# Kernel optimization log

Measured on AMD Instinct MI355X. Metric: run time of the kernel, lower is better.

The kernel has to match this reference:

```python
import jax, jax.numpy as jnp
import numpy as np

L = 512          # angles_max_length
R_CA = 3.8       # C-alpha - C-alpha virtual bond length (AB model)


def _B_mat(a, b):
    # Rigid transform of the AB C-alpha model: rot(alpha) about z, rot(beta), translate R along x.
    ca, sa = jnp.cos(a), jnp.sin(a)
    cb, sb = jnp.cos(b), jnp.sin(b)
    z = jnp.zeros_like(a)
    o = jnp.ones_like(a)
    rows = [
        [ca, -sa * cb,  sa * sb, R_CA * ca],
        [sa,  ca * cb, -ca * sb, R_CA * sa],
        [z,   sb,       cb,      z],
        [z,   z,        z,       o],
    ]
    return jnp.stack([jnp.stack(r, -1) for r in rows], -2)  # (..., 4, 4)


def _dB_da(a, b):
    ca, sa = jnp.cos(a), jnp.sin(a)
    cb, sb = jnp.cos(b), jnp.sin(b)
    z = jnp.zeros_like(a)
    rows = [
        [-sa, -ca * cb,  ca * sb, -R_CA * sa],
        [ ca, -sa * cb,  sa * sb,  R_CA * ca],
        [z, z, z, z],
        [z, z, z, z],
    ]
    return jnp.stack([jnp.stack(r, -1) for r in rows], -2)


def _dB_db(a, b):
    ca, sa = jnp.cos(a), jnp.sin(a)
    cb, sb = jnp.cos(b), jnp.sin(b)
    z = jnp.zeros_like(a)
    rows = [
        [z,  sa * sb,  sa * cb, z],
        [z, -ca * sb, -ca * cb, z],
        [z,  cb,      -sb,      z],
        [z, z, z, z],
    ]
    return jnp.stack([jnp.stack(r, -1) for r in rows], -2)


def setup_inputs() -> dict:
    key = jax.random.key(0)
    k1, k2, k3 = jax.random.split(key, 3)
    input_angles = jax.random.normal(k1, (32, 2, L), dtype=jnp.float32)
    input_coords = jax.random.normal(k2, (32, 3 * (L + 1)), dtype=jnp.float32)
    angles_length = jax.random.randint(k3, (32,), 0, L, dtype=jnp.int32)
    return {"input_angles": input_angles, "input_coords": input_coords,
            "angles_length": angles_length}


def reference(input_angles, input_coords, angles_length):
    Bsz = input_angles.shape[0]
    alpha = input_angles[:, 0, :]  # (B, L)
    beta = input_angles[:, 1, :]

    Bm = _B_mat(alpha, beta)  # (B, L, 4, 4)
    # Prefix products M_i = B_0 @ ... @ B_i (order-preserving associative scan).
    M = jax.lax.associative_scan(lambda x, y: x @ y, Bm, axis=1)
    eye = jnp.broadcast_to(jnp.eye(4, dtype=Bm.dtype), (Bsz, 1, 4, 4))
    M_prev = jnp.concatenate([eye, M[:, :-1]], axis=1)  # M_{i-1}

    # Rigid-transform inverse of M_i: [R^T, -R^T t; 0 1]
    Rm = M[..., :3, :3]
    t = M[..., :3, 3:]
    Rt = jnp.swapaxes(Rm, -1, -2)
    bottom = jnp.broadcast_to(jnp.array([0., 0., 0., 1.], Bm.dtype), (Bsz, L, 1, 4))
    Minv = jnp.concatenate(
        [jnp.concatenate([Rt, -(Rt @ t)], axis=-1), bottom], axis=-2)

    # F_i^q = M_{i-1} dB_i/dq M_i^{-1};  dr_j/dq_i = F_i^q r_j^h  (for j > i)
    Fa = M_prev @ _dB_da(alpha, beta) @ Minv  # (B, L, 4, 4)
    Fb = M_prev @ _dB_db(alpha, beta) @ Minv

    coords = input_coords.reshape(Bsz, L + 1, 3)
    rh = jnp.concatenate([coords, jnp.ones((Bsz, L + 1, 1), coords.dtype)], -1)

    ga = jnp.einsum('blij,bmj->blmi', Fa, rh)[..., :3]  # (B, L, L+1, 3)
    gb = jnp.einsum('blij,bmj->blmi', Fb, rh)[..., :3]

    i = jnp.arange(L)[:, None]
    j = jnp.arange(L + 1)[None, :]
    lens = angles_length[:, None, None]
    mask = ((j > i) & (i < lens) & (j <= lens))[..., None]
    ga = jnp.where(mask, ga, 0.0)
    gb = jnp.where(mask, gb, 0.0)

    out = jnp.stack([ga, gb], axis=1)  # (B, 2, L, L+1, 3)
    return out.reshape(Bsz, 2, 3 * L * (L + 1))
```

## Files before the change

kernel.cpp:

```cpp
#include <hip/hip_runtime.h>

#define LSEQ 512
#define RCA 3.8f

typedef float f32x4 __attribute__((ext_vector_type(4)));

struct Aff { float m[3][4]; };

__device__ __forceinline__ Aff compose(const Aff& A, const Aff& B) {
    Aff C;
#pragma unroll
    for (int i = 0; i < 3; ++i) {
#pragma unroll
        for (int j = 0; j < 4; ++j) {
            float v = A.m[i][0] * B.m[0][j] + A.m[i][1] * B.m[1][j] + A.m[i][2] * B.m[2][j];
            if (j == 3) v += A.m[i][3];
            C.m[i][j] = v;
        }
    }
    return C;
}

__device__ __forceinline__ Aff shflUp(const Aff& a, int d) {
    Aff r;
#pragma unroll
    for (int i = 0; i < 3; ++i)
#pragma unroll
        for (int j = 0; j < 4; ++j)
            r.m[i][j] = __shfl_up(a.m[i][j], d, 64);
    return r;
}

__device__ __forceinline__ Aff makeB(float ca, float sa, float cb, float sb) {
    Aff B;
    B.m[0][0] = ca;  B.m[0][1] = -sa * cb; B.m[0][2] =  sa * sb; B.m[0][3] = RCA * ca;
    B.m[1][0] = sa;  B.m[1][1] =  ca * cb; B.m[1][2] = -ca * sb; B.m[1][3] = RCA * sa;
    B.m[2][0] = 0.f; B.m[2][1] =  sb;      B.m[2][2] =  cb;      B.m[2][3] = 0.f;
    return B;
}

__global__ __launch_bounds__(512) void scan_kernel(const float* __restrict__ angles,
                                                   float* __restrict__ F) {
    const int b = blockIdx.x;
    const int tid = threadIdx.x;
    const int lane = tid & 63;
    const int w = tid >> 6;

    __shared__ float sT[8][12];

    const float a  = angles[(size_t)b * 1024 + tid];
    const float be = angles[(size_t)b * 1024 + 512 + tid];
    float sa, ca, sb, cb;
    sincosf(a, &sa, &ca);
    sincosf(be, &sb, &cb);

    Aff S = makeB(ca, sa, cb, sb);
#pragma unroll
    for (int d = 1; d < 64; d <<= 1) {
        Aff o = shflUp(S, d);
        if (lane >= d) S = compose(o, S);
    }

    if (lane == 63) {
#pragma unroll
        for (int k = 0; k < 12; ++k) sT[w][k] = S.m[k / 4][k % 4];
    }
    __syncthreads();

    Aff E;
#pragma unroll
    for (int i = 0; i < 3; ++i)
#pragma unroll
        for (int j = 0; j < 4; ++j) E.m[i][j] = (i == j) ? 1.f : 0.f;
    for (int k = 0; k < w; ++k) {
        Aff T;
#pragma unroll
        for (int q = 0; q < 12; ++q) T.m[q / 4][q % 4] = sT[k][q];
        E = compose(E, T);
    }

    const Aff Sp = shflUp(S, 1);
    const Aff M = compose(E, S);
    Aff Mprev;
    if (lane == 0) Mprev = E;
    else           Mprev = compose(E, Sp);

    float Rt[3][3], ti[3];
#pragma unroll
    for (int i = 0; i < 3; ++i)
#pragma unroll
        for (int j = 0; j < 3; ++j) Rt[i][j] = M.m[j][i];
#pragma unroll
    for (int i = 0; i < 3; ++i)
        ti[i] = -(M.m[0][i] * M.m[0][3] + M.m[1][i] * M.m[1][3] + M.m[2][i] * M.m[2][3]);

    float d0[4] = {-sa, -ca * cb,  ca * sb, -RCA * sa};
    float d1[4] = { ca, -sa * cb,  sa * sb,  RCA * ca};
    float e01 =  sa * sb, e02 =  sa * cb;
    float e11 = -ca * sb, e12 = -ca * cb;
    float e21 =  cb,      e22 = -sb;

    float Ga[3][4], Gb[3][4];
#pragma unroll
    for (int i = 0; i < 3; ++i) {
        float p0 = Mprev.m[i][0], p1 = Mprev.m[i][1], p2 = Mprev.m[i][2];
#pragma unroll
        for (int j = 0; j < 4; ++j) Ga[i][j] = p0 * d0[j] + p1 * d1[j];
        Gb[i][0] = 0.f;
        Gb[i][1] = p0 * e01 + p1 * e11 + p2 * e21;
        Gb[i][2] = p0 * e02 + p1 * e12 + p2 * e22;
        Gb[i][3] = 0.f;
    }

    float W[24];
#pragma unroll
    for (int i = 0; i < 3; ++i) {
#pragma unroll
        for (int j = 0; j < 3; ++j) {
            W[i * 4 + j]      = Ga[i][0] * Rt[0][j] + Ga[i][1] * Rt[1][j] + Ga[i][2] * Rt[2][j];
            W[12 + i * 4 + j] = Gb[i][0] * Rt[0][j] + Gb[i][1] * Rt[1][j] + Gb[i][2] * Rt[2][j];
        }
        W[i * 4 + 3]      = Ga[i][0] * ti[0] + Ga[i][1] * ti[1] + Ga[i][2] * ti[2] + Ga[i][3];
        W[12 + i * 4 + 3] = Gb[i][0] * ti[0] + Gb[i][1] * ti[1] + Gb[i][2] * ti[2] + Gb[i][3];
    }

    f32x4* w4 = reinterpret_cast<f32x4*>(F + ((size_t)b * LSEQ + tid) * 24);
    const f32x4* s4 = reinterpret_cast<const f32x4*>(W);
#pragma unroll
    for (int q = 0; q < 6; ++q) w4[q] = s4[q];
}

__global__ __launch_bounds__(256) void emit_kernel(const float* __restrict__ F,
                                                   const float* __restrict__ coords,
                                                   const int* __restrict__ lens,
                                                   float* __restrict__ out) {
    const int l = blockIdx.x;
    const int b = blockIdx.y;
    const int tid = threadIdx.x;
    int len = lens[b];
    if (len > 511) len = 511;
    const bool rowActive = (l < len);

    __shared__ float sC[1536];
    __shared__ float sF[24];

    const size_t rowA_elem = ((size_t)(b * 2) * LSEQ + l) * 1539;
    const size_t rowB_elem = rowA_elem + (size_t)LSEQ * 1539;
    float* __restrict__ rowA = out + rowA_elem;
    float* __restrict__ rowB = out + rowB_elem;
    const int h = (int)((4 - (rowA_elem & 3)) & 3);

    if (rowActive) {
        const float* cp = coords + (size_t)b * 1539;
        for (int k = tid; k < 1536; k += 256) sC[k] = cp[k];
        if (tid < 24) sF[tid] = F[((size_t)b * LSEQ + l) * 24 + tid];
        __syncthreads();
    }

    if (tid < h)     { rowA[tid] = 0.f;            rowB[tid] = 0.f; }
    if (tid < 3 - h) { rowA[h + 1536 + tid] = 0.f; rowB[h + 1536 + tid] = 0.f; }

    const int eLo = 3 * (l + 1);
    const int eHi = 3 * len + 2;

    auto doQuad = [&](int q) {
        const int p = h + 4 * q;
        f32x4 va = {0.f, 0.f, 0.f, 0.f};
        f32x4 vb = {0.f, 0.f, 0.f, 0.f};
        if (rowActive && (p + 3 >= eLo) && (p <= eHi)) {
#pragma unroll
            for (int j = 0; j < 4; ++j) {
                const int e = p + j;
                const int m = (e * 43691) >> 17;
                const int c = e - 3 * m;
                if (m > l && m <= len) {
                    const float x = sC[3 * m], y = sC[3 * m + 1], z = sC[3 * m + 2];
                    const float* fa = sF + c * 4;
                    const float* fb = fa + 12;
                    va[j] = fa[0] * x + fa[1] * y + fa[2] * z + fa[3];
                    vb[j] = fb[0] * x + fb[1] * y + fb[2] * z + fb[3];
                }
            }
        }
        __builtin_nontemporal_store(va, reinterpret_cast<f32x4*>(rowA + p));
        __builtin_nontemporal_store(vb, reinterpret_cast<f32x4*>(rowB + p));
    };

    doQuad(tid);
    if (tid < 128) doQuad(tid + 256);
}

extern "C" void kernel_launch(void* const* d_in, const int* in_sizes, int n_in,
                              void* d_out, int out_size, void* d_ws, size_t ws_size,
                              hipStream_t stream) {
    const float* angles = (const float*)d_in[0];
    const float* coords = (const float*)d_in[1];
    const int*   lens   = (const int*)d_in[2];
    float* out = (float*)d_out;
    float* F = (float*)d_ws;

    scan_kernel<<<32, 512, 0, stream>>>(angles, F);
    emit_kernel<<<dim3(512, 32), 256, 0, stream>>>(F, coords, lens, out);
}
```

Before: 228.0 us.

## Split output into bulk zero-fill kernel and active-region-only compute kernel

Adds a grid-stride zero kernel that clears the whole output with vector stores. The emit kernel is replaced by an active kernel that exits early for inactive rows and writes only the active span of each row, using scalar head and tail stores plus aligned vec4 stores. The aim is to make the fill a simple streaming write and cut compute kernel work to the triangular active region. The cost is that active elements are written twice (zero then value), nontemporal stores are dropped, and there is an extra launch.

```diff
diff --git a/kernel.cpp b/kernel.cpp
--- a/kernel.cpp
+++ b/kernel.cpp
@@ -2,6 +2,8 @@
 
 #define LSEQ 512
 #define RCA 3.8f
+#define N4 12607488
+#define PLANE_STRIDE 787968
 
 typedef float f32x4 __attribute__((ext_vector_type(4)));
 
@@ -130,64 +132,84 @@
     for (int q = 0; q < 6; ++q) w4[q] = s4[q];
 }
 
-__global__ __launch_bounds__(256) void emit_kernel(const float* __restrict__ F,
-                                                   const float* __restrict__ coords,
-                                                   const int* __restrict__ lens,
-                                                   float* __restrict__ out) {
+__global__ __launch_bounds__(256) void zero_kernel(float* __restrict__ out) {
+    f32x4* o4 = reinterpret_cast<f32x4*>(out);
+    const f32x4 z = {0.f, 0.f, 0.f, 0.f};
+    size_t i = (size_t)blockIdx.x * 256 + threadIdx.x;
+    const size_t stride = (size_t)gridDim.x * 256;
+    for (; i < N4; i += stride) o4[i] = z;
+}
+
+__global__ __launch_bounds__(256) void active_kernel(const float* __restrict__ F,
+                                                     const float* __restrict__ coords,
+                                                     const int* __restrict__ lens,
+                                                     float* __restrict__ out) {
     const int l = blockIdx.x;
     const int b = blockIdx.y;
-    const int tid = threadIdx.x;
     int len = lens[b];
     if (len > 511) len = 511;
-    const bool rowActive = (l < len);
+    if (l >= len) return;
+    const int tid = threadIdx.x;
+
+    const int sRel = 3 * (l + 1);
+    const int eRel = 3 * len + 3;
+    const int cnt  = eRel - sRel;
 
     __shared__ float sC[1536];
     __shared__ float sF[24];
 
-    const size_t rowA_elem = ((size_t)(b * 2) * LSEQ + l) * 1539;
-    const size_t rowB_elem = rowA_elem + (size_t)LSEQ * 1539;
-    float* __restrict__ rowA = out + rowA_elem;
-    float* __restrict__ rowB = out + rowB_elem;
-    const int h = (int)((4 - (rowA_elem & 3)) & 3);
-
-    if (rowActive) {
-        const float* cp = coords + (size_t)b * 1539;
-        for (int k = tid; k < 1536; k += 256) sC[k] = cp[k];
-        if (tid < 24) sF[tid] = F[((size_t)b * LSEQ + l) * 24 + tid];
-        __syncthreads();
-    }
-
-    if (tid < h)     { rowA[tid] = 0.f;            rowB[tid] = 0.f; }
-    if (tid < 3 - h) { rowA[h + 1536 + tid] = 0.f; rowB[h + 1536 + tid] = 0.f; }
-
-    const int eLo = 3 * (l + 1);
-    const int eHi = 3 * len + 2;
-
-    auto doQuad = [&](int q) {
-        const int p = h + 4 * q;
-        f32x4 va = {0.f, 0.f, 0.f, 0.f};
-        f32x4 vb = {0.f, 0.f, 0.f, 0.f};
-        if (rowActive && (p + 3 >= eLo) && (p <= eHi)) {
-#pragma unroll
-            for (int j = 0; j < 4; ++j) {
-                const int e = p + j;
-                const int m = (e * 43691) >> 17;
-                const int c = e - 3 * m;
-                if (m > l && m <= len) {
-                    const float x = sC[3 * m], y = sC[3 * m + 1], z = sC[3 * m + 2];
-                    const float* fa = sF + c * 4;
-                    const float* fb = fa + 12;
-                    va[j] = fa[0] * x + fa[1] * y + fa[2] * z + fa[3];
-                    vb[j] = fb[0] * x + fb[1] * y + fb[2] * z + fb[3];
-                }
-            }
-        }
-        __builtin_nontemporal_store(va, reinterpret_cast<f32x4*>(rowA + p));
-        __builtin_nontemporal_store(vb, reinterpret_cast<f32x4*>(rowB + p));
+    const float* cp = coords + (size_t)b * 1539 + sRel;
+    for (int k = tid; k < cnt; k += 256) sC[k] = cp[k];
+    if (tid < 24) sF[tid] = F[((size_t)b * LSEQ + l) * 24 + tid];
+    __syncthreads();
+
+    const size_t base0 = ((size_t)(b * 2) * LSEQ + l) * 1539;
+    const size_t sAbs = base0 + sRel;
+    const size_t eAbs = base0 + eRel;
+    size_t qs = (sAbs + 3) & ~(size_t)3; if (qs > eAbs) qs = eAbs;
+    size_t qe = eAbs & ~(size_t)3;       if (qe < qs)  qe = qs;
+
+    auto compute = [&](int rr, float& va, float& vb) {
+        const int m = (rr * 43691) >> 17;
+        const int c = rr - 3 * m;
+        const int o = 3 * m - sRel;
+        const float x = sC[o], y = sC[o + 1], z = sC[o + 2];
+        const float* fa = sF + c * 4;
+        const float* fb = fa + 12;
+        va = fa[0] * x + fa[1] * y + fa[2] * z + fa[3];
+        vb = fb[0] * x + fb[1] * y + fb[2] * z + fb[3];
     };
 
-    doQuad(tid);
-    if (tid < 128) doQuad(tid + 256);
+    {
+        const int n = (int)(qs - sAbs);
+        if (tid < n) {
+            float va, vb; compute(sRel + tid, va, vb);
+            out[sAbs + tid] = va;
+            out[sAbs + tid + PLANE_STRIDE] = vb;
+        }
+    }
+    {
+        const int n = (int)(eAbs - qe);
+        if (tid < n) {
+            const int rr = (int)(qe - base0) + tid;
+            float va, vb; compute(rr, va, vb);
+            out[qe + tid] = va;
+            out[qe + tid + PLANE_STRIDE] = vb;
+        }
+    }
+    const int nq = (int)((qe - qs) >> 2);
+    for (int q = tid; q < nq; q += 256) {
+        const size_t abs0 = qs + 4 * (size_t)q;
+        const int rr0 = (int)(abs0 - base0);
+        f32x4 va, vb;
+#pragma unroll
+        for (int j = 0; j < 4; ++j) {
+            float a, bb; compute(rr0 + j, a, bb);
+            va[j] = a; vb[j] = bb;
+        }
+        *reinterpret_cast<f32x4*>(out + abs0) = va;
+        *reinterpret_cast<f32x4*>(out + abs0 + PLANE_STRIDE) = vb;
+    }
 }
 
 extern "C" void kernel_launch(void* const* d_in, const int* in_sizes, int n_in,
@@ -199,6 +221,7 @@
     float* out = (float*)d_out;
     float* F = (float*)d_ws;
 
+    zero_kernel<<<2048, 256, 0, stream>>>(out);
     scan_kernel<<<32, 512, 0, stream>>>(angles, F);
-    emit_kernel<<<dim3(512, 32), 256, 0, stream>>>(F, coords, lens, out);
-}
+    active_kernel<<<dim3(512, 32), 256, 0, stream>>>(F, coords, lens, out);
+}
```

Measured after the change: 223.1 us. 1.02x faster.

## Rewrite emit kernel as flat grid-stride tiled writer over output

Applied to the files above, without the earlier changes.

The emit kernel no longer uses one block per row with shared-memory staging. It now treats the output as a flat array of 256-element tiles, each handled by one wavefront in a persistent grid-stride loop. Each tile is checked for whether it touches any active row region, and if not it writes zeros without loads. Active elements read F and coords directly from global memory (cache) instead of LDS, and the stores are now aligned and no longer nontemporal. This aims to remove per-block setup, synchronisation and unaligned row-edge handling, at the cost of per-element index math and uncached-by-LDS scattered loads.

```diff
diff --git a/kernel.cpp b/kernel.cpp
--- a/kernel.cpp
+++ b/kernel.cpp
@@ -2,6 +2,9 @@
 
 #define LSEQ 512
 #define RCA 3.8f
+#define NROWS 32768
+#define ROWLEN 1539
+#define NTILES 196992
 
 typedef float f32x4 __attribute__((ext_vector_type(4)));
 
@@ -134,60 +137,60 @@
                                                    const float* __restrict__ coords,
                                                    const int* __restrict__ lens,
                                                    float* __restrict__ out) {
-    const int l = blockIdx.x;
-    const int b = blockIdx.y;
-    const int tid = threadIdx.x;
-    int len = lens[b];
-    if (len > 511) len = 511;
-    const bool rowActive = (l < len);
-
-    __shared__ float sC[1536];
-    __shared__ float sF[24];
-
-    const size_t rowA_elem = ((size_t)(b * 2) * LSEQ + l) * 1539;
-    const size_t rowB_elem = rowA_elem + (size_t)LSEQ * 1539;
-    float* __restrict__ rowA = out + rowA_elem;
-    float* __restrict__ rowB = out + rowB_elem;
-    const int h = (int)((4 - (rowA_elem & 3)) & 3);
-
-    if (rowActive) {
-        const float* cp = coords + (size_t)b * 1539;
-        for (int k = tid; k < 1536; k += 256) sC[k] = cp[k];
-        if (tid < 24) sF[tid] = F[((size_t)b * LSEQ + l) * 24 + tid];
-        __syncthreads();
-    }
-
-    if (tid < h)     { rowA[tid] = 0.f;            rowB[tid] = 0.f; }
-    if (tid < 3 - h) { rowA[h + 1536 + tid] = 0.f; rowB[h + 1536 + tid] = 0.f; }
-
-    const int eLo = 3 * (l + 1);
-    const int eHi = 3 * len + 2;
-
-    auto doQuad = [&](int q) {
-        const int p = h + 4 * q;
-        f32x4 va = {0.f, 0.f, 0.f, 0.f};
-        f32x4 vb = {0.f, 0.f, 0.f, 0.f};
-        if (rowActive && (p + 3 >= eLo) && (p <= eHi)) {
-#pragma unroll
-            for (int j = 0; j < 4; ++j) {
-                const int e = p + j;
-                const int m = (e * 43691) >> 17;
-                const int c = e - 3 * m;
-                if (m > l && m <= len) {
-                    const float x = sC[3 * m], y = sC[3 * m + 1], z = sC[3 * m + 2];
-                    const float* fa = sF + c * 4;
-                    const float* fb = fa + 12;
-                    va[j] = fa[0] * x + fa[1] * y + fa[2] * z + fa[3];
-                    vb[j] = fb[0] * x + fb[1] * y + fb[2] * z + fb[3];
+    const int lane = threadIdx.x & 63;
+    int wid0 = blockIdx.x * 4 + (threadIdx.x >> 6);
+    wid0 = __builtin_amdgcn_readfirstlane(wid0);
+    const int nW = gridDim.x * 4;
+
+    for (int t = wid0; t < NTILES; t += nW) {
+        const long long Tel = (long long)t * 256;
+        const int r0   = (int)(((unsigned long long)Tel * 1428865014ull) >> 41);
+        const int relT = (int)(Tel - (long long)r0 * ROWLEN);
+        const bool spill = (relT + 256 > ROWLEN);
+
+        bool act = false;
+        {
+            const int l0 = r0 & 511, b0 = r0 >> 10;
+            int len0 = lens[b0]; if (len0 > 511) len0 = 511;
+            if (l0 < len0) {
+                const int lo = 3 * (l0 + 1), hi = 3 * len0 + 3;
+                const int e0 = spill ? ROWLEN : relT + 256;
+                act = (relT < hi) && (e0 > lo);
+            }
+            if (!act && spill) {
+                const int r1 = r0 + 1;
+                const int l1 = r1 & 511, b1 = r1 >> 10;
+                int len1 = lens[b1]; if (len1 > 511) len1 = 511;
+                if (l1 < len1) {
+                    const int lo = 3 * (l1 + 1);
+                    const int e1 = relT + 256 - ROWLEN;
+                    act = (e1 > lo);
                 }
             }
         }
-        __builtin_nontemporal_store(va, reinterpret_cast<f32x4*>(rowA + p));
-        __builtin_nontemporal_store(vb, reinterpret_cast<f32x4*>(rowB + p));
-    };
-
-    doQuad(tid);
-    if (tid < 128) doQuad(tid + 256);
+
+        f32x4 v = {0.f, 0.f, 0.f, 0.f};
+        if (act) {
+            const int relLane = relT + lane * 4;
+#pragma unroll
+            for (int j = 0; j < 4; ++j) {
+                int rel = relLane + j;
+                const bool c1 = (rel >= ROWLEN);
+                const int row = c1 ? r0 + 1 : r0;
+                if (c1) rel -= ROWLEN;
+                const int l = row & 511, b = row >> 10, plane = (row >> 9) & 1;
+                int len = lens[b]; if (len > 511) len = 511;
+                if (l < len && rel >= 3 * (l + 1) && rel < 3 * len + 3) {
+                    const int m = (rel * 43691) >> 17;
+                    const int c = rel - 3 * m;
+                    const float* fa = F + ((size_t)(b * 512 + l)) * 24 + plane * 12 + c * 4;
+                    const float* cp = coords + (size_t)b * ROWLEN + 3 * m;
+                    v[j] = fa[0] * cp[0] + fa[1] * cp[1] + fa[2] * cp[2] + fa[3];
+                }
+            }
+        }
+        *reinterpret_cast<f32x4*>(out + Tel + lane * 4) = v;
+    }
 }
 
 extern "C" void kernel_launch(void* const* d_in, const int* in_sizes, int n_in,
@@ -200,5 +203,5 @@
     float* F = (float*)d_ws;
 
     scan_kernel<<<32, 512, 0, stream>>>(angles, F);
-    emit_kernel<<<dim3(512, 32), 256, 0, stream>>>(F, coords, lens, out);
-}
+    emit_kernel<<<8192, 256, 0, stream>>>(F, coords, lens, out);
+}
```

Result: faster. 211.2 us (-7.4%).
